# Optimization experiments

Hardware: AMD Instinct MI355X
Metric: run time of the kernel (lower is better)

The kernel has to match this reference:

```python
import jax, jax.numpy as jnp
import numpy as np

N_HEADS = 71
HEAD_DIM = 64
ROPE_BASE = 10000.0
SCALE = 1.0 / np.sqrt(HEAD_DIM)  # 0.125


def setup_inputs() -> dict:
    key = jax.random.key(0)
    k1, k2, k3 = jax.random.split(key, 3)
    B, S, H = 1, 1024, N_HEADS * HEAD_DIM  # 4544
    F = (N_HEADS + 2) * HEAD_DIM           # 4672 fused QKV out features
    hidden_states = jax.random.normal(k1, (B, 1, S, H), dtype=jnp.float32)
    qkv_weight = jax.random.normal(k2, (H, F), dtype=jnp.float32) * 0.02
    dense_weight = jax.random.normal(k3, (H, H), dtype=jnp.float32) * 0.02
    # additive causal mask [1,1,S,S]
    causal = np.tril(np.ones((S, S), dtype=bool))
    attention_mask = jnp.asarray(np.where(causal, 0.0, -1e9).astype(np.float32))[None, None]
    return {"hidden_states": hidden_states, "qkv_weight": qkv_weight,
            "dense_weight": dense_weight, "attention_mask": attention_mask}


def _rope_tables(seq_len):
    inv_freq = 1.0 / (ROPE_BASE ** (jnp.arange(0, HEAD_DIM, 2, dtype=jnp.float32) / HEAD_DIM))
    t = jnp.arange(seq_len, dtype=jnp.float32)
    freqs = t[:, None] * inv_freq[None, :]          # [S, 32]
    emb = jnp.concatenate([freqs, freqs], axis=-1)  # [S, 64]
    return jnp.cos(emb), jnp.sin(emb)


def _rotate_half(x):
    h = HEAD_DIM // 2
    return jnp.concatenate([-x[..., h:], x[..., :h]], axis=-1)


def reference(hidden_states, qkv_weight, dense_weight, attention_mask):
    # Prefill: hidden_states [B, 1, S, H]
    B, _, S, H = hidden_states.shape
    x = hidden_states[:, 0]                                  # [B, S, H]
    qkv = jnp.einsum('bsh,hf->bsf', x, qkv_weight)           # fused QKV matmul
    qd = N_HEADS * HEAD_DIM
    # Falcon-7B MQA head split: 71 query heads, 1 shared K and V head
    q = qkv[..., :qd].reshape(B, S, N_HEADS, HEAD_DIM).transpose(0, 2, 1, 3)  # [B, nH, S, d]
    k = qkv[..., qd:qd + HEAD_DIM]                           # [B, S, d]
    v = qkv[..., qd + HEAD_DIM:]                             # [B, S, d]
    cos, sin = _rope_tables(S)                               # [S, d]
    q = q * cos + _rotate_half(q) * sin
    k = k * cos + _rotate_half(k) * sin
    scores = jnp.einsum('bhqd,bkd->bhqk', q, k) * SCALE      # [B, nH, S, S]
    scores = scores + attention_mask                         # causal mask (alibi is None for Falcon-7B)
    probs = jax.nn.softmax(scores, axis=-1)
    ctx = jnp.einsum('bhqk,bkd->bhqd', probs, v)             # [B, nH, S, d]
    merged = ctx.transpose(0, 2, 1, 3).reshape(B, S, H)      # concat heads
    out = jnp.einsum('bsh,hf->bsf', merged, dense_weight)    # selfout dense
    return out[:, None]                                      # [B, 1, S, H]
```

## Files before the change

### kernel.cpp

```cpp
#include <hip/hip_runtime.h>
#include <hip/hip_bf16.h>

#define DI __device__ __forceinline__

typedef __attribute__((ext_vector_type(8))) short bf16x8;
typedef __attribute__((ext_vector_type(4))) float f32x4;
typedef __attribute__((ext_vector_type(4))) short s16x4;

constexpr int S  = 1024;
constexpr int NH = 71;
constexpr int HD = 64;
constexpr int H  = NH * HD;
constexpr int F  = (NH + 2) * HD;
constexpr float K2 = 0.125f * 1.44269504f;

DI short f2bf(float f) {
  union { float f; unsigned u; } v; v.f = f;
  unsigned r = v.u + 0x7fffu + ((v.u >> 16) & 1u);
  return (short)(r >> 16);
}
DI unsigned cvt_pk_bf16(float lo, float hi) {
  unsigned r;
  asm("v_cvt_pk_bf16_f32 %0, %1, %2" : "=v"(r) : "v"(lo), "v"(hi));
  return r;
}
DI float redmax_g(float x) {
  float y = fmaxf(x, __int_as_float(__builtin_amdgcn_ds_swizzle(__float_as_int(x), 0x401F)));
  return fmaxf(y, __shfl_xor(y, 32));
}
DI float redsum_g(float x) {
  float y = x + __int_as_float(__builtin_amdgcn_ds_swizzle(__float_as_int(x), 0x401F));
  return y + __shfl_xor(y, 32);
}

DI void gload_lds16(const void* g, void* l) {
  __builtin_amdgcn_global_load_lds(
      (const __attribute__((address_space(1))) unsigned int*)g,
      (__attribute__((address_space(3))) unsigned int*)l, 16, 0, 0);
}

DI bf16x8 ldswz(const char* base, int row, int slot) {
  return *(const bf16x8*)(base + row * 128 + ((slot ^ (row & 7)) << 4));
}

__global__ void cast_x_kernel(const float* __restrict__ x, short* __restrict__ xb, int n4) {
  int i = blockIdx.x * blockDim.x + threadIdx.x;
  if (i >= n4) return;
  f32x4 v = ((const f32x4*)x)[i];
  s16x4 o = { f2bf(v.x), f2bf(v.y), f2bf(v.z), f2bf(v.w) };
  ((s16x4*)xb)[i] = o;
}

__global__ __launch_bounds__(256) void transpose_cast_kernel(
    const float* __restrict__ W, short* __restrict__ Wt, int K, int N) {
  __shared__ float tile[64][65];
  int n0 = blockIdx.x * 64, k0 = blockIdx.y * 64;
  int c = threadIdx.x & 63, rg = threadIdx.x >> 6;
#pragma unroll
  for (int i = 0; i < 16; ++i) {
    int r = rg * 16 + i;
    tile[r][c] = W[(size_t)(k0 + r) * N + n0 + c];
  }
  __syncthreads();
#pragma unroll
  for (int i = 0; i < 16; ++i) {
    int r = rg * 16 + i;
    Wt[(size_t)(n0 + r) * K + k0 + c] = f2bf(tile[c][r]);
  }
}

__global__ void rope_tables_kernel(float* __restrict__ ct, float* __restrict__ st) {
  int s = blockIdx.x, i = threadIdx.x;
  float invf = powf(10000.0f, -(float)i / 32.0f);
  float a = (float)s * invf;
  ct[s * 32 + i] = cosf(a);
  st[s * 32 + i] = sinf(a);
}

__global__ __launch_bounds__(256) void rope_pack_kernel(
    const float* __restrict__ qkv, const float* __restrict__ ct, const float* __restrict__ st,
    short* __restrict__ Qb, short* __restrict__ Kb, short* __restrict__ Vt) {
  int s = blockIdx.x;
  const float* row = qkv + (size_t)s * F;
  for (int c = threadIdx.x; c < F; c += 256) {
    int hh = c >> 6, d = c & 63;
    float v = row[c];
    if (hh <= NH) {
      int i = d & 31;
      float cs = ct[s * 32 + i], sn = st[s * 32 + i];
      float rot = (d < 32) ? -row[c + 32] : row[c - 32];
      short ob = f2bf(v * cs + rot * sn);
      if (hh < NH) Qb[((size_t)hh * S + s) * 64 + d] = ob;
      else         Kb[(size_t)s * 64 + d] = ob;
    } else {
      Vt[(size_t)d * S + s] = f2bf(v);
    }
  }
}

__global__ __launch_bounds__(256, 3) void gemm_bt_kernel(
    const short* __restrict__ A, const short* __restrict__ Bt, float* __restrict__ C,
    int M, int N, int K) {
  __shared__ short As[2 * 128 * 64];
  __shared__ short Bs[2 * 64 * 64];
  const int tid = threadIdx.x;
  const int lane = tid & 63;
  const int wave = tid >> 6;
  const int wr = wave >> 1, wc = wave & 1;
  const int lr = lane & 15, g = lane >> 4;

  const int nwg = gridDim.x;
  int bid = blockIdx.x;
  int wgid = ((nwg & 7) == 0) ? ((bid & 7) * (nwg >> 3) + (bid >> 3)) : bid;
  const int ntm = M >> 7;
  const int tn = wgid / ntm;
  const int tm = wgid % ntm;

  f32x4 acc[4][2] = {};

  int srowA[4], skofA[4];
#pragma unroll
  for (int iss = 0; iss < 4; ++iss) {
    int d = iss * 256 + wave * 64 + lane;
    int row = (d >> 2) & 127;
    int c = (d & 3) ^ ((row >> 1) & 3);
    srowA[iss] = row;
    skofA[iss] = ((d >> 9) << 5) + c * 8;
  }
  int srowB[2], skofB[2];
#pragma unroll
  for (int iss = 0; iss < 2; ++iss) {
    int d = iss * 256 + wave * 64 + lane;
    int row = (d >> 2) & 63;
    int c = (d & 3) ^ ((row >> 1) & 3);
    srowB[iss] = row;
    skofB[iss] = ((d >> 8) << 5) + c * 8;
  }
  int offA[2][4], offB[2][2];
#pragma unroll
  for (int im = 0; im < 4; ++im) {
    int row_a = wr * 64 + im * 16 + lr;
    int sl = (g ^ ((row_a >> 1) & 3)) << 4;
#pragma unroll
    for (int kk = 0; kk < 2; ++kk) offA[kk][im] = kk * 8192 + row_a * 64 + sl;
  }
#pragma unroll
  for (int in = 0; in < 2; ++in) {
    int row_b = wc * 32 + in * 16 + lr;
    int sl = (g ^ ((row_b >> 1) & 3)) << 4;
#pragma unroll
    for (int kk = 0; kk < 2; ++kk) offB[kk][in] = kk * 4096 + row_b * 64 + sl;
  }

  char* AsB = (char*)As;
  char* BsB = (char*)Bs;
  const size_t Abase = (size_t)tm * 128 * K;
  const size_t Bbase = (size_t)tn * 64 * K;

#define STAGE(buf, k0)                                                                  \
  {                                                                                     \
    _Pragma("unroll")                                                                   \
    for (int iss = 0; iss < 4; ++iss)                                                   \
      gload_lds16(A + Abase + (size_t)srowA[iss] * K + (k0) + skofA[iss],               \
                  AsB + (buf) * 16384 + (iss * 4 + wave) * 1024);                       \
    _Pragma("unroll")                                                                   \
    for (int iss = 0; iss < 2; ++iss)                                                   \
      gload_lds16(Bt + Bbase + (size_t)srowB[iss] * K + (k0) + skofB[iss],              \
                  BsB + (buf) * 8192 + (iss * 4 + wave) * 1024);                        \
  }

  STAGE(0, 0);
  __syncthreads();
  const int KS = K >> 6;
  for (int t = 0; t < KS; ++t) {
    const int cur = t & 1;
    if (t + 1 < KS) STAGE(cur ^ 1, (t + 1) << 6);
    const char* Ac = AsB + cur * 16384;
    const char* Bc = BsB + cur * 8192;
    bf16x8 af[2][4], bfr[2][2];
#pragma unroll
    for (int kk = 0; kk < 2; ++kk) {
#pragma unroll
      for (int im = 0; im < 4; ++im) af[kk][im] = *(const bf16x8*)(Ac + offA[kk][im]);
#pragma unroll
      for (int in = 0; in < 2; ++in) bfr[kk][in] = *(const bf16x8*)(Bc + offB[kk][in]);
    }
#pragma unroll
    for (int kk = 0; kk < 2; ++kk)
#pragma unroll
      for (int im = 0; im < 4; ++im)
#pragma unroll
        for (int in = 0; in < 2; ++in)
          acc[im][in] = __builtin_amdgcn_mfma_f32_16x16x32_bf16(af[kk][im], bfr[kk][in], acc[im][in], 0, 0, 0);
    __syncthreads();
  }
#undef STAGE

#pragma unroll
  for (int im = 0; im < 4; ++im) {
#pragma unroll
    for (int in = 0; in < 2; ++in) {
      int row = tm * 128 + wr * 64 + im * 16 + g * 4;
      int col = tn * 64 + wc * 32 + in * 16 + lr;
#pragma unroll
      for (int i = 0; i < 4; ++i)
        C[(size_t)(row + i) * N + col] = acc[im][in][i];
    }
  }
}

DI void attn_step(const char* Kc, const char* Vc, char* P,
                  int key0, int qrow, bf16x8 aQ0, bf16x8 aQ1,
                  f32x4* accO, float& m, float& l, int lr, int g) {
  f32x4 p[4];
#pragma unroll
  for (int nf = 0; nf < 4; ++nf) {
    int row = nf * 16 + lr;
    bf16x8 k0 = ldswz(Kc, row, g);
    bf16x8 k1 = ldswz(Kc, row, g + 4);
    f32x4 z = {};
    z = __builtin_amdgcn_mfma_f32_16x16x32_bf16(k0, aQ0, z, 0, 0, 0);
    p[nf] = __builtin_amdgcn_mfma_f32_16x16x32_bf16(k1, aQ1, z, 0, 0, 0);
  }
  float pmx = -3e30f;
#pragma unroll
  for (int nf = 0; nf < 4; ++nf)
#pragma unroll
    for (int i = 0; i < 4; ++i) {
      int key = key0 + nf * 16 + 4 * g + i;
      float sv = p[nf][i] * K2 + (key <= qrow ? 0.0f : -1e30f);
      p[nf][i] = sv;
      pmx = fmaxf(pmx, sv);
    }
  float pm = redmax_g(pmx);
  float mn = fmaxf(m, pm);
  float scl = __builtin_exp2f(m - mn);
  m = mn;
  float rsx = 0.f;
#pragma unroll
  for (int nf = 0; nf < 4; ++nf) {
    f32x4 pe;
#pragma unroll
    for (int i = 0; i < 4; ++i) {
      pe[i] = __builtin_exp2f(p[nf][i] - m);
      rsx += pe[i];
    }
    uint2 wv;
    wv.x = cvt_pk_bf16(pe[0], pe[1]);
    wv.y = cvt_pk_bf16(pe[2], pe[3]);
    *(uint2*)(P + lr * 144 + nf * 32 + g * 8) = wv;
  }
  float rs = redsum_g(rsx);
  l = l * scl + rs;
#pragma unroll
  for (int df = 0; df < 4; ++df)
#pragma unroll
    for (int i = 0; i < 4; ++i)
      accO[df][i] *= scl;
#pragma unroll
  for (int st = 0; st < 2; ++st) {
    bf16x8 bP = *(const bf16x8*)(P + lr * 144 + st * 64 + g * 16);
#pragma unroll
    for (int df = 0; df < 4; ++df) {
      bf16x8 aV = ldswz(Vc, df * 16 + lr, g + 4 * st);
      accO[df] = __builtin_amdgcn_mfma_f32_16x16x32_bf16(aV, bP, accO[df], 0, 0, 0);
    }
  }
}

__global__ __launch_bounds__(256) void attn_kernel(
    const short* __restrict__ Qb,
    const short* __restrict__ Kb,
    const short* __restrict__ Vt,
    short* __restrict__ merged) {
  __shared__ short Ks[2][4096];
  __shared__ short Vs[2][4096];
  __shared__ short Ps[4][16 * 72];
  const int lane = threadIdx.x & 63, w = threadIdx.x >> 6;
  const int lr = lane & 15, g = lane >> 4;
  const int j = blockIdx.x, head = blockIdx.y;
  const int kbmax = 15 - j;
  const int qA = j * 64 + w * 16 + lr;
  const int qB = (15 - j) * 64 + w * 16 + lr;
  char* KsB = (char*)Ks;
  char* VsB = (char*)Vs;
  char* P = (char*)Ps[w];

  int crow[2], cslot[2];
#pragma unroll
  for (int i = 0; i < 2; ++i) {
    int c = (i * 4 + w) * 64 + lane;
    crow[i] = c >> 3;
    cslot[i] = (c & 7) ^ (crow[i] & 7);
  }

  const short* qap = Qb + ((size_t)head * S + qA) * 64 + g * 8;
  bf16x8 aQA0 = *(const bf16x8*)(qap);
  bf16x8 aQA1 = *(const bf16x8*)(qap + 32);
  const short* qbp = Qb + ((size_t)head * S + qB) * 64 + g * 8;
  bf16x8 aQB0 = *(const bf16x8*)(qbp);
  bf16x8 aQB1 = *(const bf16x8*)(qbp + 32);

  f32x4 accA[4] = {}, accB[4] = {};
  float mA = -3e30f, lA = 0.f, mB = -3e30f, lB = 0.f;

#define STAGEKV(buf, key0)                                                       \
  {                                                                              \
    _Pragma("unroll")                                                            \
    for (int i = 0; i < 2; ++i) {                                                \
      gload_lds16(Kb + (size_t)((key0) + crow[i]) * 64 + cslot[i] * 8,           \
                  KsB + (buf) * 8192 + (i * 4 + w) * 1024);                      \
      gload_lds16(Vt + (size_t)crow[i] * S + (key0) + cslot[i] * 8,              \
                  VsB + (buf) * 8192 + (i * 4 + w) * 1024);                      \
    }                                                                            \
  }

  STAGEKV(0, 0);
  for (int kb = 0; kb <= kbmax; ++kb) {
    const int cur = kb & 1;
    __syncthreads();
    if (kb < kbmax) STAGEKV(cur ^ 1, (kb + 1) * 64);
    const char* Kc = KsB + cur * 8192;
    const char* Vc = VsB + cur * 8192;
    attn_step(Kc, Vc, P, kb * 64, qB, aQB0, aQB1, accB, mB, lB, lr, g);
    if (kb <= j)
      attn_step(Kc, Vc, P, kb * 64, qA, aQA0, aQA1, accA, mA, lA, lr, g);
  }
#undef STAGEKV

  float rlA = 1.0f / lA, rlB = 1.0f / lB;
#pragma unroll
  for (int df = 0; df < 4; ++df)
#pragma unroll
    for (int i = 0; i < 4; ++i) {
      int d = head * 64 + df * 16 + 4 * g + i;
      merged[(size_t)qB * H + d] = f2bf(accB[df][i] * rlB);
      merged[(size_t)qA * H + d] = f2bf(accA[df][i] * rlA);
    }
}

extern "C" void kernel_launch(void* const* d_in, const int* in_sizes, int n_in,
                              void* d_out, int out_size, void* d_ws, size_t ws_size,
                              hipStream_t stream) {
  const float* x    = (const float*)d_in[0];
  const float* wqkv = (const float*)d_in[1];
  const float* wd   = (const float*)d_in[2];
  float* out = (float*)d_out;

  char* ws = (char*)d_ws;
  size_t off = 0;
  short* Wqkvt  = (short*)(ws + off); off += (size_t)F * H * 2;
  short* Wdt    = (short*)(ws + off); off += (size_t)H * H * 2;
  short* Qb     = (short*)(ws + off); off += (size_t)NH * S * HD * 2;
  short* Kb     = (short*)(ws + off); off += (size_t)S * HD * 2;
  short* Vtb    = (short*)(ws + off); off += (size_t)HD * S * 2;
  short* merged = (short*)(ws + off); off += (size_t)S * H * 2;
  float* ct     = (float*)(ws + off); off += (size_t)S * 32 * 4;
  float* st     = (float*)(ws + off); off += (size_t)S * 32 * 4;
  short* xb     = (short*)(ws + off); off += (size_t)S * H * 2;
  float* qkv    = (float*)(ws + off); off += (size_t)S * F * 4;
  (void)ws_size; (void)in_sizes; (void)n_in; (void)out_size;

  hipLaunchKernelGGL(cast_x_kernel, dim3((S * H / 4 + 255) / 256), dim3(256), 0, stream,
                     x, xb, S * H / 4);
  hipLaunchKernelGGL(transpose_cast_kernel, dim3(F / 64, H / 64), dim3(256), 0, stream,
                     wqkv, Wqkvt, H, F);
  hipLaunchKernelGGL(transpose_cast_kernel, dim3(H / 64, H / 64), dim3(256), 0, stream,
                     wd, Wdt, H, H);
  hipLaunchKernelGGL(rope_tables_kernel, dim3(S), dim3(32), 0, stream, ct, st);
  hipLaunchKernelGGL(gemm_bt_kernel, dim3((F / 64) * (S / 128)), dim3(256), 0, stream,
                     xb, Wqkvt, qkv, S, F, H);
  hipLaunchKernelGGL(rope_pack_kernel, dim3(S), dim3(256), 0, stream,
                     qkv, ct, st, Qb, Kb, Vtb);
  hipLaunchKernelGGL(attn_kernel, dim3(8, NH), dim3(256), 0, stream,
                     Qb, Kb, Vtb, merged);
  hipLaunchKernelGGL(gemm_bt_kernel, dim3((H / 64) * (S / 128)), dim3(256), 0, stream,
                     merged, Wdt, out, S, H, H);
}
```

Measured before the change: 239.6 us.

## Fuse weight fp32-to-bf16 transpose cast into GEMM B-operand loading

Removes the two standalone transpose_cast kernels. The GEMM now reads the fp32 weights directly into registers, converts them to packed bf16 and writes them into the swizzled LDS B tile, with register double-buffering and explicit waitcnt/barrier scheduling. This avoids writing and re-reading a bf16 copy of both weight matrices in HBM and saves two launches. In exchange each GEMM tile re-reads fp32 weights (twice the bytes of bf16) once per M tile, and the B path now goes through VGPRs instead of direct global-to-LDS loads, which adds register pressure.

```diff
diff --git a/kernel.cpp b/kernel.cpp
--- a/kernel.cpp
+++ b/kernel.cpp
@@ -49,24 +49,6 @@
   f32x4 v = ((const f32x4*)x)[i];
   s16x4 o = { f2bf(v.x), f2bf(v.y), f2bf(v.z), f2bf(v.w) };
   ((s16x4*)xb)[i] = o;
-}
-
-__global__ __launch_bounds__(256) void transpose_cast_kernel(
-    const float* __restrict__ W, short* __restrict__ Wt, int K, int N) {
-  __shared__ float tile[64][65];
-  int n0 = blockIdx.x * 64, k0 = blockIdx.y * 64;
-  int c = threadIdx.x & 63, rg = threadIdx.x >> 6;
-#pragma unroll
-  for (int i = 0; i < 16; ++i) {
-    int r = rg * 16 + i;
-    tile[r][c] = W[(size_t)(k0 + r) * N + n0 + c];
-  }
-  __syncthreads();
-#pragma unroll
-  for (int i = 0; i < 16; ++i) {
-    int r = rg * 16 + i;
-    Wt[(size_t)(n0 + r) * K + k0 + c] = f2bf(tile[c][r]);
-  }
 }
 
 __global__ void rope_tables_kernel(float* __restrict__ ct, float* __restrict__ st) {
@@ -98,8 +80,8 @@
   }
 }
 
-__global__ __launch_bounds__(256, 3) void gemm_bt_kernel(
-    const short* __restrict__ A, const short* __restrict__ Bt, float* __restrict__ C,
+__global__ __launch_bounds__(256, 3) void gemm_fb_kernel(
+    const short* __restrict__ A, const float* __restrict__ W, float* __restrict__ C,
     int M, int N, int K) {
   __shared__ short As[2 * 128 * 64];
   __shared__ short Bs[2 * 64 * 64];
@@ -127,14 +109,15 @@
     srowA[iss] = row;
     skofA[iss] = ((d >> 9) << 5) + c * 8;
   }
-  int srowB[2], skofB[2];
-#pragma unroll
-  for (int iss = 0; iss < 2; ++iss) {
-    int d = iss * 256 + wave * 64 + lane;
-    int row = (d >> 2) & 63;
-    int c = (d & 3) ^ ((row >> 1) & 3);
-    srowB[iss] = row;
-    skofB[iss] = ((d >> 8) << 5) + c * 8;
+  const int nq = tid & 15;
+  const int kr = tid >> 4;
+  const int bn0 = tn * 64 + 4 * nq;
+  int wB[4];
+#pragma unroll
+  for (int j = 0; j < 4; ++j) {
+    int n = 4 * nq + j;
+    wB[j] = (kr >> 3) * 4096 + n * 64 +
+            ((((kr >> 1) & 3) ^ ((n >> 1) & 3)) << 4) + (kr & 1) * 8;
   }
   int offA[2][4], offB[2][2];
 #pragma unroll
@@ -155,46 +138,72 @@
   char* AsB = (char*)As;
   char* BsB = (char*)Bs;
   const size_t Abase = (size_t)tm * 128 * K;
-  const size_t Bbase = (size_t)tn * 64 * K;
-
-#define STAGE(buf, k0)                                                                  \
-  {                                                                                     \
-    _Pragma("unroll")                                                                   \
-    for (int iss = 0; iss < 4; ++iss)                                                   \
-      gload_lds16(A + Abase + (size_t)srowA[iss] * K + (k0) + skofA[iss],               \
-                  AsB + (buf) * 16384 + (iss * 4 + wave) * 1024);                       \
-    _Pragma("unroll")                                                                   \
-    for (int iss = 0; iss < 2; ++iss)                                                   \
-      gload_lds16(Bt + Bbase + (size_t)srowB[iss] * K + (k0) + skofB[iss],              \
-                  BsB + (buf) * 8192 + (iss * 4 + wave) * 1024);                        \
-  }
-
-  STAGE(0, 0);
-  __syncthreads();
+
+  f32x4 rB0[4], rB1[4];
+
+#define LOADB(R, t)                                                              \
+  { _Pragma("unroll")                                                            \
+    for (int i = 0; i < 4; ++i)                                                  \
+      R[i] = *(const f32x4*)(W + (size_t)((t) * 64 + 4 * kr + i) * N + bn0); }
+
+#define GLOADA(buf, t)                                                           \
+  { _Pragma("unroll")                                                            \
+    for (int iss = 0; iss < 4; ++iss)                                            \
+      gload_lds16(A + Abase + (size_t)srowA[iss] * K + ((t) << 6) + skofA[iss],  \
+                  AsB + (buf) * 16384 + (iss * 4 + wave) * 1024); }
+
+#define KBODY(curb, Rc, Rn, t, last)                                             \
+  {                                                                              \
+    if (!(last)) LOADB(Rn, (t) + 1);                                             \
+    if (!(last)) asm volatile("s_waitcnt vmcnt(4)" ::: "memory");                \
+    else         asm volatile("s_waitcnt vmcnt(0)" ::: "memory");                \
+    __builtin_amdgcn_sched_barrier(0);                                           \
+    _Pragma("unroll")                                                            \
+    for (int j = 0; j < 4; ++j) {                                                \
+      uint2 wv;                                                                  \
+      wv.x = cvt_pk_bf16(Rc[0][j], Rc[1][j]);                                    \
+      wv.y = cvt_pk_bf16(Rc[2][j], Rc[3][j]);                                    \
+      *(uint2*)(BsB + (curb) * 8192 + wB[j]) = wv;                               \
+    }                                                                            \
+    asm volatile("s_waitcnt lgkmcnt(0)" ::: "memory");                           \
+    __builtin_amdgcn_sched_barrier(0);                                           \
+    __builtin_amdgcn_s_barrier();                                                \
+    __builtin_amdgcn_sched_barrier(0);                                           \
+    if (!(last)) GLOADA((curb) ^ 1, (t) + 1);                                    \
+    const char* Ac = AsB + (curb) * 16384;                                       \
+    const char* Bc = BsB + (curb) * 8192;                                        \
+    bf16x8 af[2][4], bfr[2][2];                                                  \
+    _Pragma("unroll")                                                            \
+    for (int kk = 0; kk < 2; ++kk) {                                             \
+      _Pragma("unroll")                                                          \
+      for (int im = 0; im < 4; ++im) af[kk][im] = *(const bf16x8*)(Ac + offA[kk][im]); \
+      _Pragma("unroll")                                                          \
+      for (int in = 0; in < 2; ++in) bfr[kk][in] = *(const bf16x8*)(Bc + offB[kk][in]); \
+    }                                                                            \
+    __builtin_amdgcn_s_setprio(1);                                               \
+    _Pragma("unroll")                                                            \
+    for (int kk = 0; kk < 2; ++kk)                                               \
+      _Pragma("unroll")                                                          \
+      for (int im = 0; im < 4; ++im)                                             \
+        _Pragma("unroll")                                                        \
+        for (int in = 0; in < 2; ++in)                                           \
+          acc[im][in] = __builtin_amdgcn_mfma_f32_16x16x32_bf16(af[kk][im], bfr[kk][in], acc[im][in], 0, 0, 0); \
+    __builtin_amdgcn_s_setprio(0);                                               \
+  }
+
   const int KS = K >> 6;
-  for (int t = 0; t < KS; ++t) {
-    const int cur = t & 1;
-    if (t + 1 < KS) STAGE(cur ^ 1, (t + 1) << 6);
-    const char* Ac = AsB + cur * 16384;
-    const char* Bc = BsB + cur * 8192;
-    bf16x8 af[2][4], bfr[2][2];
-#pragma unroll
-    for (int kk = 0; kk < 2; ++kk) {
-#pragma unroll
-      for (int im = 0; im < 4; ++im) af[kk][im] = *(const bf16x8*)(Ac + offA[kk][im]);
-#pragma unroll
-      for (int in = 0; in < 2; ++in) bfr[kk][in] = *(const bf16x8*)(Bc + offB[kk][in]);
-    }
-#pragma unroll
-    for (int kk = 0; kk < 2; ++kk)
-#pragma unroll
-      for (int im = 0; im < 4; ++im)
-#pragma unroll
-        for (int in = 0; in < 2; ++in)
-          acc[im][in] = __builtin_amdgcn_mfma_f32_16x16x32_bf16(af[kk][im], bfr[kk][in], acc[im][in], 0, 0, 0);
-    __syncthreads();
-  }
-#undef STAGE
+  LOADB(rB0, 0);
+  GLOADA(0, 0);
+  int t = 0;
+  for (; t + 2 < KS; t += 2) {
+    KBODY(0, rB0, rB1, t, false);
+    KBODY(1, rB1, rB0, t + 1, false);
+  }
+  KBODY(0, rB0, rB1, t, true);
+
+#undef KBODY
+#undef GLOADA
+#undef LOADB
 
 #pragma unroll
   for (int im = 0; im < 4; ++im) {
@@ -349,8 +358,6 @@
 
   char* ws = (char*)d_ws;
   size_t off = 0;
-  short* Wqkvt  = (short*)(ws + off); off += (size_t)F * H * 2;
-  short* Wdt    = (short*)(ws + off); off += (size_t)H * H * 2;
   short* Qb     = (short*)(ws + off); off += (size_t)NH * S * HD * 2;
   short* Kb     = (short*)(ws + off); off += (size_t)S * HD * 2;
   short* Vtb    = (short*)(ws + off); off += (size_t)HD * S * 2;
@@ -363,17 +370,13 @@
 
   hipLaunchKernelGGL(cast_x_kernel, dim3((S * H / 4 + 255) / 256), dim3(256), 0, stream,
                      x, xb, S * H / 4);
-  hipLaunchKernelGGL(transpose_cast_kernel, dim3(F / 64, H / 64), dim3(256), 0, stream,
-                     wqkv, Wqkvt, H, F);
-  hipLaunchKernelGGL(transpose_cast_kernel, dim3(H / 64, H / 64), dim3(256), 0, stream,
-                     wd, Wdt, H, H);
   hipLaunchKernelGGL(rope_tables_kernel, dim3(S), dim3(32), 0, stream, ct, st);
-  hipLaunchKernelGGL(gemm_bt_kernel, dim3((F / 64) * (S / 128)), dim3(256), 0, stream,
-                     xb, Wqkvt, qkv, S, F, H);
+  hipLaunchKernelGGL(gemm_fb_kernel, dim3((F / 64) * (S / 128)), dim3(256), 0, stream,
+                     xb, wqkv, qkv, S, F, H);
   hipLaunchKernelGGL(rope_pack_kernel, dim3(S), dim3(256), 0, stream,
                      qkv, ct, st, Qb, Kb, Vtb);
   hipLaunchKernelGGL(attn_kernel, dim3(8, NH), dim3(256), 0, stream,
                      Qb, Kb, Vtb, merged);
-  hipLaunchKernelGGL(gemm_bt_kernel, dim3((H / 64) * (S / 128)), dim3(256), 0, stream,
-                     merged, Wdt, out, S, H, H);
-}
+  hipLaunchKernelGGL(gemm_fb_kernel, dim3((H / 64) * (S / 128)), dim3(256), 0, stream,
+                     merged, wd, out, S, H, H);
+}
```

Measured after the change: 292.0 us. +21.9%, slower.
